# Kernel tuning notes

Hardware: AMD Instinct MI355X
Metric: run time of the kernel (lower is better)

## Reference

```python
import jax, jax.numpy as jnp
import numpy as np

N = 50000      # nodes
E = 800000     # random edges (self-loops appended -> E + N total)
IN, HID, OUT, HEADS = 128, 256, 256, 8


def _gat_layer(x, src, dst, W, a_src, a_dst, bias):
    # x: [N, F_in]; W: [F_in, H*C]; a_src/a_dst: [H, C]; bias: [H*C]
    n = x.shape[0]
    H, C = a_src.shape
    h = (x @ W).reshape(n, H, C)                      # per-head transform
    al_s = jnp.sum(h * a_src, axis=-1)                # [N, H]
    al_d = jnp.sum(h * a_dst, axis=-1)                # [N, H]
    e = jax.nn.leaky_relu(al_s[src] + al_d[dst], 0.2) # [E, H]
    # segmented softmax over incoming edges of each destination node
    m = jax.ops.segment_max(e, dst, num_segments=n)   # [N, H]
    e = jnp.exp(e - m[dst])
    s = jax.ops.segment_sum(e, dst, num_segments=n)   # [N, H]
    alpha = e / (s[dst] + 1e-16)                      # [E, H]
    out = jax.ops.segment_sum(alpha[:, :, None] * h[src], dst, num_segments=n)
    return out.reshape(n, H * C) + bias


def setup_inputs() -> dict:
    key = jax.random.key(0)
    ks = jax.random.split(key, 9)
    x = jax.random.normal(ks[0], (N, IN), dtype=jnp.float32)
    src = jax.random.randint(ks[1], (E,), 0, N)
    dst = jax.random.randint(ks[2], (E,), 0, N)
    loop = jnp.arange(N)  # PyG GATConv adds self-loops by default
    edge_index = jnp.stack([jnp.concatenate([src, loop]),
                            jnp.concatenate([dst, loop])]).astype(jnp.int64)
    C1, C2 = HID // HEADS, OUT // HEADS
    W1 = jax.random.normal(ks[3], (IN, HID), jnp.float32) * (1.0 / np.sqrt(IN))
    a1_src = jax.random.normal(ks[4], (HEADS, C1), jnp.float32) * 0.1
    a1_dst = jax.random.normal(ks[5], (HEADS, C1), jnp.float32) * 0.1
    b1 = jnp.zeros((HID,), jnp.float32)
    W2 = jax.random.normal(ks[6], (HID, OUT), jnp.float32) * (1.0 / np.sqrt(HID))
    a2_src = jax.random.normal(ks[7], (HEADS, C2), jnp.float32) * 0.1
    a2_dst = jax.random.normal(ks[8], (HEADS, C2), jnp.float32) * 0.1
    b2 = jnp.zeros((OUT,), jnp.float32)
    return {"x": x, "edge_index": edge_index,
            "W1": W1, "a1_src": a1_src, "a1_dst": a1_dst, "b1": b1,
            "W2": W2, "a2_src": a2_src, "a2_dst": a2_dst, "b2": b2}


def reference(x, edge_index, W1, a1_src, a1_dst, b1, W2, a2_src, a2_dst, b2):
    src, dst = edge_index[0], edge_index[1]
    h = jax.nn.elu(_gat_layer(x, src, dst, W1, a1_src, a1_dst, b1))
    out = jax.nn.elu(_gat_layer(h, src, dst, W2, a2_src, a2_dst, b2))
    return out
```

## Files before the change

kernel.cpp:

```cpp
#include <hip/hip_runtime.h>
#include <hip/hip_bf16.h>


#define HEADS 8
#define F 256

typedef _Float16 h8 __attribute__((ext_vector_type(8)));
typedef _Float16 h4 __attribute__((ext_vector_type(4)));
typedef float f4 __attribute__((ext_vector_type(4)));

#define WAVE_SYNC() do { __builtin_amdgcn_wave_barrier(); \
  asm volatile("s_waitcnt lgkmcnt(0)" ::: "memory"); \
  __builtin_amdgcn_wave_barrier(); } while (0)


__global__ void k_cvt(const float* __restrict__ in, _Float16* __restrict__ out, int n) {
  int i = blockIdx.x * blockDim.x + threadIdx.x;
  int idx = i * 4;
  if (idx < n) {
    float4 v = *(const float4*)&in[idx];
    h4 o = {(_Float16)v.x, (_Float16)v.y, (_Float16)v.z, (_Float16)v.w};
    *(h4*)&out[idx] = o;
  }
}

__global__ void k_cvt_wt(const float* __restrict__ W, _Float16* __restrict__ Wt, int K) {
  int k = blockIdx.x, n = threadIdx.x;
  Wt[(size_t)n * K + k] = (_Float16)W[(size_t)k * F + n];
}


__global__ void k_hist(const int* __restrict__ dst, int Et, int* __restrict__ deg) {
  int i = blockIdx.x * blockDim.x + threadIdx.x;
  if (i < Et) atomicAdd(&deg[dst[i]], 1);
}

__global__ __launch_bounds__(1024) void k_scan1(const int* __restrict__ deg, int n,
                                                int* __restrict__ rowptr, int* __restrict__ bsum) {
  __shared__ int s[1024];
  int i = blockIdx.x * 1024 + threadIdx.x;
  int v = (i < n) ? deg[i] : 0;
  s[threadIdx.x] = v;
  __syncthreads();
  for (int off = 1; off < 1024; off <<= 1) {
    int add = (threadIdx.x >= off) ? s[threadIdx.x - off] : 0;
    __syncthreads();
    s[threadIdx.x] += add;
    __syncthreads();
  }
  if (i < n) rowptr[i] = s[threadIdx.x] - v;
  if (threadIdx.x == 1023) bsum[blockIdx.x] = s[1023];
}

__global__ void k_scan2(const int* __restrict__ bsum, int nb, int* __restrict__ boff) {
  int t = threadIdx.x;
  int v = (t < nb) ? bsum[t] : 0;
  int inc = v;
  for (int off = 1; off < 64; off <<= 1) {
    int y = __shfl_up(inc, off, 64);
    if (t >= off) inc += y;
  }
  boff[t] = inc - v;
}

__global__ void k_scan3(int n, int Et, int* __restrict__ rowptr, const int* __restrict__ boff) {
  int i = blockIdx.x * blockDim.x + threadIdx.x;
  if (i < n) rowptr[i] += boff[i >> 10];
  if (i == 0) rowptr[n] = Et;
}

__global__ void k_fill(const int* __restrict__ src, const int* __restrict__ dst, int Et,
                       const int* __restrict__ rowptr, int* __restrict__ fill,
                       int* __restrict__ csr_src) {
  int i = blockIdx.x * blockDim.x + threadIdx.x;
  if (i < Et) {
    int d = dst[i];
    int pos = rowptr[d] + atomicAdd(&fill[d], 1);
    csr_src[pos] = src[i];
  }
}


__global__ __launch_bounds__(256) void k_gemm(const _Float16* __restrict__ A,
                                              const _Float16* __restrict__ Bt,
                                              _Float16* __restrict__ C,
                                              const float* __restrict__ a_src,
                                              const float* __restrict__ a_dst,
                                              float* __restrict__ als,
                                              float* __restrict__ ald,
                                              int M, int K) {
  __shared__ _Float16 As[64][40];
  __shared__ _Float16 Bs[256][40];
  int tid = threadIdx.x;
  int lane = tid & 63, w = tid >> 6;
  int rowBase = blockIdx.x * 64;
  f4 acc[4][4] = {};

  int arow = tid >> 2, akoff = (tid & 3) * 8;
  int arow_g = min(rowBase + arow, M - 1);
  const _Float16* Ap = A + (size_t)arow_g * K + akoff;
  const _Float16* Bp = Bt + (size_t)tid * K;

  int kl = (lane >> 4) * 8;
  int rl = lane & 15;

  for (int k0 = 0; k0 < K; k0 += 32) {
    h8 av = *(const h8*)(Ap + k0);
    h8 bv0 = *(const h8*)(Bp + k0);
    h8 bv1 = *(const h8*)(Bp + k0 + 8);
    h8 bv2 = *(const h8*)(Bp + k0 + 16);
    h8 bv3 = *(const h8*)(Bp + k0 + 24);
    *(h8*)&As[arow][akoff] = av;
    *(h8*)&Bs[tid][0] = bv0;
    *(h8*)&Bs[tid][8] = bv1;
    *(h8*)&Bs[tid][16] = bv2;
    *(h8*)&Bs[tid][24] = bv3;
    __syncthreads();
    h8 af[4], bf[4];
#pragma unroll
    for (int fi = 0; fi < 4; ++fi) af[fi] = *(const h8*)&As[fi * 16 + rl][kl];
#pragma unroll
    for (int fj = 0; fj < 4; ++fj) bf[fj] = *(const h8*)&Bs[w * 64 + fj * 16 + rl][kl];
#pragma unroll
    for (int fi = 0; fi < 4; ++fi)
#pragma unroll
      for (int fj = 0; fj < 4; ++fj)
        acc[fi][fj] = __builtin_amdgcn_mfma_f32_16x16x32_f16(af[fi], bf[fj], acc[fi][fj], 0, 0, 0);
    __syncthreads();
  }

  int rquad = (lane >> 4) * 4;

#pragma unroll
  for (int fi = 0; fi < 4; ++fi)
#pragma unroll
    for (int fj = 0; fj < 4; ++fj) {
      int col = w * 64 + fj * 16 + rl;
#pragma unroll
      for (int r = 0; r < 4; ++r) {
        int row = rowBase + fi * 16 + rquad + r;
        if (row < M) C[(size_t)row * F + col] = (_Float16)acc[fi][fj][r];
      }
    }

  int head0 = w * 2;
  float as0 = a_src[head0 * 32 + rl],      as1 = a_src[head0 * 32 + 16 + rl];
  float ad0 = a_dst[head0 * 32 + rl],      ad1 = a_dst[head0 * 32 + 16 + rl];
  float cs0 = a_src[head0 * 32 + 32 + rl], cs1 = a_src[head0 * 32 + 48 + rl];
  float cd0 = a_dst[head0 * 32 + 32 + rl], cd1 = a_dst[head0 * 32 + 48 + rl];
#pragma unroll
  for (int fi = 0; fi < 4; ++fi)
#pragma unroll
    for (int r = 0; r < 4; ++r) {
      float v0s = acc[fi][0][r] * as0 + acc[fi][1][r] * as1;
      float v0d = acc[fi][0][r] * ad0 + acc[fi][1][r] * ad1;
      float v1s = acc[fi][2][r] * cs0 + acc[fi][3][r] * cs1;
      float v1d = acc[fi][2][r] * cd0 + acc[fi][3][r] * cd1;
#pragma unroll
      for (int off = 8; off; off >>= 1) {
        v0s += __shfl_xor(v0s, off);
        v0d += __shfl_xor(v0d, off);
        v1s += __shfl_xor(v1s, off);
        v1d += __shfl_xor(v1d, off);
      }
      int row = rowBase + fi * 16 + rquad + r;
      if (rl == 0 && row < M) {
        als[row * HEADS + head0] = v0s;
        ald[row * HEADS + head0] = v0d;
        als[row * HEADS + head0 + 1] = v1s;
        ald[row * HEADS + head0 + 1] = v1d;
      }
    }
}


template <bool F16OUT>
__global__ __launch_bounds__(256) void k_agg(const int* __restrict__ rowptr,
                                             const int* __restrict__ csr_src,
                                             const float* __restrict__ al_s,
                                             const float* __restrict__ al_d,
                                             const _Float16* __restrict__ h,
                                             const float* __restrict__ bias,
                                             float* __restrict__ outf,
                                             _Float16* __restrict__ outh,
                                             int n) {
  __shared__ float eps[4][64][8];
  __shared__ int ssrc[4][64];
  int tid = threadIdx.x;
  int w = tid >> 6, lane = tid & 63;
  int node = blockIdx.x * 4 + w;
  if (node >= n) return;
  int base = rowptr[node];
  int d = rowptr[node + 1] - base;
  int hh = lane >> 3, slot = lane & 7;
  float alD = al_d[node * HEADS + hh];

  float invs;
  f4 facc = {0.f, 0.f, 0.f, 0.f};
  const _Float16* hc = h + (lane << 2);

  if (d <= 64) {
    float m = -1e30f;
    for (int j = slot; j < d; j += 8) {
      int s = csr_src[base + j];
      if (hh == 0) ssrc[w][j] = s;
      float e = al_s[s * HEADS + hh] + alD;
      e = (e > 0.f) ? e : 0.2f * e;
      eps[w][j][hh] = e;
      m = fmaxf(m, e);
    }
#pragma unroll
    for (int off = 4; off; off >>= 1) m = fmaxf(m, __shfl_xor(m, off));
    float sm = 0.f;
    for (int j = slot; j < d; j += 8) {
      float p = __expf(eps[w][j][hh] - m);
      eps[w][j][hh] = p;
      sm += p;
    }
#pragma unroll
    for (int off = 4; off; off >>= 1) sm += __shfl_xor(sm, off);
    invs = 1.f / (sm + 1e-16f);
    WAVE_SYNC();
    int j = 0;
    for (; j + 4 <= d; j += 4) {
      int s0 = __builtin_amdgcn_readfirstlane(ssrc[w][j]);
      int s1 = __builtin_amdgcn_readfirstlane(ssrc[w][j + 1]);
      int s2 = __builtin_amdgcn_readfirstlane(ssrc[w][j + 2]);
      int s3 = __builtin_amdgcn_readfirstlane(ssrc[w][j + 3]);
      float p0 = eps[w][j][hh], p1 = eps[w][j + 1][hh];
      float p2 = eps[w][j + 2][hh], p3 = eps[w][j + 3][hh];
      h4 v0 = *(const h4*)(hc + ((size_t)s0 << 8));
      h4 v1 = *(const h4*)(hc + ((size_t)s1 << 8));
      h4 v2 = *(const h4*)(hc + ((size_t)s2 << 8));
      h4 v3 = *(const h4*)(hc + ((size_t)s3 << 8));
      facc.x += p0 * (float)v0.x + p1 * (float)v1.x + p2 * (float)v2.x + p3 * (float)v3.x;
      facc.y += p0 * (float)v0.y + p1 * (float)v1.y + p2 * (float)v2.y + p3 * (float)v3.y;
      facc.z += p0 * (float)v0.z + p1 * (float)v1.z + p2 * (float)v2.z + p3 * (float)v3.z;
      facc.w += p0 * (float)v0.w + p1 * (float)v1.w + p2 * (float)v2.w + p3 * (float)v3.w;
    }
    for (; j < d; ++j) {
      int s0 = __builtin_amdgcn_readfirstlane(ssrc[w][j]);
      float p0 = eps[w][j][hh];
      h4 v0 = *(const h4*)(hc + ((size_t)s0 << 8));
      facc.x += p0 * (float)v0.x;
      facc.y += p0 * (float)v0.y;
      facc.z += p0 * (float)v0.z;
      facc.w += p0 * (float)v0.w;
    }
  } else {
    float m = -1e30f;
    for (int j = slot; j < d; j += 8) {
      int s = csr_src[base + j];
      float e = al_s[s * HEADS + hh] + alD;
      e = (e > 0.f) ? e : 0.2f * e;
      m = fmaxf(m, e);
    }
#pragma unroll
    for (int off = 4; off; off >>= 1) m = fmaxf(m, __shfl_xor(m, off));
    float sm = 0.f;
    for (int j = slot; j < d; j += 8) {
      int s = csr_src[base + j];
      float e = al_s[s * HEADS + hh] + alD;
      e = (e > 0.f) ? e : 0.2f * e;
      sm += __expf(e - m);
    }
#pragma unroll
    for (int off = 4; off; off >>= 1) sm += __shfl_xor(sm, off);
    invs = 1.f / (sm + 1e-16f);
    for (int c0 = 0; c0 < d; c0 += 64) {
      int cn = min(64, d - c0);
      WAVE_SYNC();
      for (int j = slot; j < cn; j += 8) {
        int s = csr_src[base + c0 + j];
        if (hh == 0) ssrc[w][j] = s;
        float e = al_s[s * HEADS + hh] + alD;
        e = (e > 0.f) ? e : 0.2f * e;
        eps[w][j][hh] = __expf(e - m);
      }
      WAVE_SYNC();
      for (int j = 0; j < cn; ++j) {
        int s0 = __builtin_amdgcn_readfirstlane(ssrc[w][j]);
        float p0 = eps[w][j][hh];
        h4 v0 = *(const h4*)(hc + ((size_t)s0 << 8));
        facc.x += p0 * (float)v0.x;
        facc.y += p0 * (float)v0.y;
        facc.z += p0 * (float)v0.z;
        facc.w += p0 * (float)v0.w;
      }
    }
  }

  int c0 = lane << 2;
  float4 bv = *(const float4*)&bias[c0];
  float o0 = facc.x * invs + bv.x;
  float o1 = facc.y * invs + bv.y;
  float o2 = facc.z * invs + bv.z;
  float o3 = facc.w * invs + bv.w;
  o0 = (o0 > 0.f) ? o0 : expm1f(o0);
  o1 = (o1 > 0.f) ? o1 : expm1f(o1);
  o2 = (o2 > 0.f) ? o2 : expm1f(o2);
  o3 = (o3 > 0.f) ? o3 : expm1f(o3);
  if (F16OUT) {
    h4 o = {(_Float16)o0, (_Float16)o1, (_Float16)o2, (_Float16)o3};
    *(h4*)&outh[((size_t)node << 8) + c0] = o;
  } else {
    *(float4*)&outf[((size_t)node << 8) + c0] = make_float4(o0, o1, o2, o3);
  }
}


extern "C" void kernel_launch(void* const* d_in, const int* in_sizes, int n_in,
                              void* d_out, int out_size, void* d_ws, size_t ws_size,
                              hipStream_t stream) {
  const float* x   = (const float*)d_in[0];
  const int*   ei  = (const int*)d_in[1];
  const float* W1  = (const float*)d_in[2];
  const float* a1s = (const float*)d_in[3];
  const float* a1d = (const float*)d_in[4];
  const float* b1  = (const float*)d_in[5];
  const float* W2  = (const float*)d_in[6];
  const float* a2s = (const float*)d_in[7];
  const float* a2d = (const float*)d_in[8];
  const float* b2  = (const float*)d_in[9];

  int n  = in_sizes[0] / 128;
  int Et = in_sizes[1] / 2;
  const int* srcp = ei;
  const int* dstp = ei + Et;

  char* ws = (char*)d_ws;
  auto alloc = [&](size_t bytes) {
    char* p = ws;
    ws += (bytes + 255) & ~(size_t)255;
    return p;
  };
  _Float16* xh     = (_Float16*)alloc((size_t)n * 128 * 2);
  _Float16* hbuf   = (_Float16*)alloc((size_t)n * F * 2);
  _Float16* Wt1    = (_Float16*)alloc((size_t)128 * F * 2);
  _Float16* Wt2    = (_Float16*)alloc((size_t)F * F * 2);
  float*    als    = (float*)alloc((size_t)n * HEADS * 4);
  float*    ald    = (float*)alloc((size_t)n * HEADS * 4);
  int*      deg    = (int*)alloc((size_t)n * 4);
  int*      fill   = (int*)alloc((size_t)n * 4);
  int*      rowptr = (int*)alloc((size_t)(n + 1) * 4);
  int*      bsum   = (int*)alloc(64 * 4);
  int*      boff   = (int*)alloc(64 * 4);
  int*      csr    = (int*)alloc((size_t)Et * 4);
  _Float16* out1h  = (_Float16*)d_out;
  float*    outF   = (float*)d_out;

  hipMemsetAsync(deg, 0, (size_t)n * 4, stream);
  hipMemsetAsync(fill, 0, (size_t)n * 4, stream);

  k_cvt<<<(n * 128 / 4 + 255) / 256, 256, 0, stream>>>(x, xh, n * 128);
  k_cvt_wt<<<128, 256, 0, stream>>>(W1, Wt1, 128);
  k_cvt_wt<<<256, 256, 0, stream>>>(W2, Wt2, 256);

  int eb = (Et + 255) / 256;
  k_hist<<<eb, 256, 0, stream>>>(dstp, Et, deg);
  int nb = (n + 1023) / 1024;
  k_scan1<<<nb, 1024, 0, stream>>>(deg, n, rowptr, bsum);
  k_scan2<<<1, 64, 0, stream>>>(bsum, nb, boff);
  k_scan3<<<(n + 255) / 256, 256, 0, stream>>>(n, Et, rowptr, boff);
  k_fill<<<eb, 256, 0, stream>>>(srcp, dstp, Et, rowptr, fill, csr);

  int gb = (n + 63) / 64;
  int ab = (n + 3) / 4;
  k_gemm<<<gb, 256, 0, stream>>>(xh, Wt1, hbuf, a1s, a1d, als, ald, n, 128);
  k_agg<true><<<ab, 256, 0, stream>>>(rowptr, csr, als, ald, hbuf, b1, nullptr, out1h, n);
  k_gemm<<<gb, 256, 0, stream>>>(out1h, Wt2, hbuf, a2s, a2d, als, ald, n, 256);
  k_agg<false><<<ab, 256, 0, stream>>>(rowptr, csr, als, ald, hbuf, b2, outF, nullptr, n);
}
```

Before: 395.3 us.

## Split attention aggregation into alpha and gather kernels, prefetch GEMM tiles

Splits the fused softmax+aggregation kernel into a kernel that writes normalized fp16 attention weights per edge and a separate gather kernel that reads them. It also register-prefetches the next K tile in the GEMM, merges the two weight-transpose launches, and drops the fill counter by atomically bumping a copy of rowptr. The split adds an extra Et*8 fp16 write and read per layer plus an extra launch. The fp16 alpha slightly reduces precision.

```diff
diff --git a/kernel.cpp b/kernel.cpp
--- a/kernel.cpp
+++ b/kernel.cpp
@@ -8,10 +8,6 @@
 typedef _Float16 h8 __attribute__((ext_vector_type(8)));
 typedef _Float16 h4 __attribute__((ext_vector_type(4)));
 typedef float f4 __attribute__((ext_vector_type(4)));
-
-#define WAVE_SYNC() do { __builtin_amdgcn_wave_barrier(); \
-  asm volatile("s_waitcnt lgkmcnt(0)" ::: "memory"); \
-  __builtin_amdgcn_wave_barrier(); } while (0)
 
 
 __global__ void k_cvt(const float* __restrict__ in, _Float16* __restrict__ out, int n) {
@@ -24,9 +20,14 @@
   }
 }
 
-__global__ void k_cvt_wt(const float* __restrict__ W, _Float16* __restrict__ Wt, int K) {
-  int k = blockIdx.x, n = threadIdx.x;
-  Wt[(size_t)n * K + k] = (_Float16)W[(size_t)k * F + n];
+__global__ void k_cvt_wt2(const float* __restrict__ W1, _Float16* __restrict__ Wt1,
+                          const float* __restrict__ W2, _Float16* __restrict__ Wt2) {
+  int b = blockIdx.x, n = threadIdx.x;
+  if (b < 128) Wt1[(size_t)n * 128 + b] = (_Float16)W1[(size_t)b * F + n];
+  else {
+    int k = b - 128;
+    Wt2[(size_t)n * 256 + k] = (_Float16)W2[(size_t)k * F + n];
+  }
 }
 
 
@@ -63,19 +64,22 @@
   boff[t] = inc - v;
 }
 
-__global__ void k_scan3(int n, int Et, int* __restrict__ rowptr, const int* __restrict__ boff) {
+__global__ void k_scan3(int n, int Et, int* __restrict__ rowptr,
+                        int* __restrict__ rowwork, const int* __restrict__ boff) {
   int i = blockIdx.x * blockDim.x + threadIdx.x;
-  if (i < n) rowptr[i] += boff[i >> 10];
+  if (i < n) {
+    int v = rowptr[i] + boff[i >> 10];
+    rowptr[i] = v;
+    rowwork[i] = v;
+  }
   if (i == 0) rowptr[n] = Et;
 }
 
 __global__ void k_fill(const int* __restrict__ src, const int* __restrict__ dst, int Et,
-                       const int* __restrict__ rowptr, int* __restrict__ fill,
-                       int* __restrict__ csr_src) {
+                       int* __restrict__ rowwork, int* __restrict__ csr_src) {
   int i = blockIdx.x * blockDim.x + threadIdx.x;
   if (i < Et) {
-    int d = dst[i];
-    int pos = rowptr[d] + atomicAdd(&fill[d], 1);
+    int pos = atomicAdd(&rowwork[dst[i]], 1);
     csr_src[pos] = src[i];
   }
 }
@@ -104,18 +108,28 @@
   int kl = (lane >> 4) * 8;
   int rl = lane & 15;
 
-  for (int k0 = 0; k0 < K; k0 += 32) {
-    h8 av = *(const h8*)(Ap + k0);
-    h8 bv0 = *(const h8*)(Bp + k0);
-    h8 bv1 = *(const h8*)(Bp + k0 + 8);
-    h8 bv2 = *(const h8*)(Bp + k0 + 16);
-    h8 bv3 = *(const h8*)(Bp + k0 + 24);
+  int nsteps = K >> 5;
+  h8 av = *(const h8*)(Ap);
+  h8 bv0 = *(const h8*)(Bp);
+  h8 bv1 = *(const h8*)(Bp + 8);
+  h8 bv2 = *(const h8*)(Bp + 16);
+  h8 bv3 = *(const h8*)(Bp + 24);
+
+  for (int s = 0; s < nsteps; ++s) {
     *(h8*)&As[arow][akoff] = av;
     *(h8*)&Bs[tid][0] = bv0;
     *(h8*)&Bs[tid][8] = bv1;
     *(h8*)&Bs[tid][16] = bv2;
     *(h8*)&Bs[tid][24] = bv3;
     __syncthreads();
+    if (s + 1 < nsteps) {
+      int k0 = (s + 1) << 5;
+      av = *(const h8*)(Ap + k0);
+      bv0 = *(const h8*)(Bp + k0);
+      bv1 = *(const h8*)(Bp + k0 + 8);
+      bv2 = *(const h8*)(Bp + k0 + 16);
+      bv3 = *(const h8*)(Bp + k0 + 24);
+    }
     h8 af[4], bf[4];
 #pragma unroll
     for (int fi = 0; fi < 4; ++fi) af[fi] = *(const h8*)&As[fi * 16 + rl][kl];
@@ -174,18 +188,13 @@
 }
 
 
-template <bool F16OUT>
-__global__ __launch_bounds__(256) void k_agg(const int* __restrict__ rowptr,
-                                             const int* __restrict__ csr_src,
-                                             const float* __restrict__ al_s,
-                                             const float* __restrict__ al_d,
-                                             const _Float16* __restrict__ h,
-                                             const float* __restrict__ bias,
-                                             float* __restrict__ outf,
-                                             _Float16* __restrict__ outh,
-                                             int n) {
+__global__ __launch_bounds__(256) void k_alpha(const int* __restrict__ rowptr,
+                                               const int* __restrict__ csr_src,
+                                               const float* __restrict__ al_s,
+                                               const float* __restrict__ al_d,
+                                               _Float16* __restrict__ alpha,
+                                               int n) {
   __shared__ float eps[4][64][8];
-  __shared__ int ssrc[4][64];
   int tid = threadIdx.x;
   int w = tid >> 6, lane = tid & 63;
   int node = blockIdx.x * 4 + w;
@@ -195,15 +204,10 @@
   int hh = lane >> 3, slot = lane & 7;
   float alD = al_d[node * HEADS + hh];
 
-  float invs;
-  f4 facc = {0.f, 0.f, 0.f, 0.f};
-  const _Float16* hc = h + (lane << 2);
-
   if (d <= 64) {
     float m = -1e30f;
     for (int j = slot; j < d; j += 8) {
       int s = csr_src[base + j];
-      if (hh == 0) ssrc[w][j] = s;
       float e = al_s[s * HEADS + hh] + alD;
       e = (e > 0.f) ? e : 0.2f * e;
       eps[w][j][hh] = e;
@@ -219,34 +223,9 @@
     }
 #pragma unroll
     for (int off = 4; off; off >>= 1) sm += __shfl_xor(sm, off);
-    invs = 1.f / (sm + 1e-16f);
-    WAVE_SYNC();
-    int j = 0;
-    for (; j + 4 <= d; j += 4) {
-      int s0 = __builtin_amdgcn_readfirstlane(ssrc[w][j]);
-      int s1 = __builtin_amdgcn_readfirstlane(ssrc[w][j + 1]);
-      int s2 = __builtin_amdgcn_readfirstlane(ssrc[w][j + 2]);
-      int s3 = __builtin_amdgcn_readfirstlane(ssrc[w][j + 3]);
-      float p0 = eps[w][j][hh], p1 = eps[w][j + 1][hh];
-      float p2 = eps[w][j + 2][hh], p3 = eps[w][j + 3][hh];
-      h4 v0 = *(const h4*)(hc + ((size_t)s0 << 8));
-      h4 v1 = *(const h4*)(hc + ((size_t)s1 << 8));
-      h4 v2 = *(const h4*)(hc + ((size_t)s2 << 8));
-      h4 v3 = *(const h4*)(hc + ((size_t)s3 << 8));
-      facc.x += p0 * (float)v0.x + p1 * (float)v1.x + p2 * (float)v2.x + p3 * (float)v3.x;
-      facc.y += p0 * (float)v0.y + p1 * (float)v1.y + p2 * (float)v2.y + p3 * (float)v3.y;
-      facc.z += p0 * (float)v0.z + p1 * (float)v1.z + p2 * (float)v2.z + p3 * (float)v3.z;
-      facc.w += p0 * (float)v0.w + p1 * (float)v1.w + p2 * (float)v2.w + p3 * (float)v3.w;
-    }
-    for (; j < d; ++j) {
-      int s0 = __builtin_amdgcn_readfirstlane(ssrc[w][j]);
-      float p0 = eps[w][j][hh];
-      h4 v0 = *(const h4*)(hc + ((size_t)s0 << 8));
-      facc.x += p0 * (float)v0.x;
-      facc.y += p0 * (float)v0.y;
-      facc.z += p0 * (float)v0.z;
-      facc.w += p0 * (float)v0.w;
-    }
+    float invs = 1.f / (sm + 1e-16f);
+    for (int j = slot; j < d; j += 8)
+      alpha[(size_t)(base + j) * 8 + hh] = (_Float16)(eps[w][j][hh] * invs);
   } else {
     float m = -1e30f;
     for (int j = slot; j < d; j += 8) {
@@ -266,36 +245,74 @@
     }
 #pragma unroll
     for (int off = 4; off; off >>= 1) sm += __shfl_xor(sm, off);
-    invs = 1.f / (sm + 1e-16f);
-    for (int c0 = 0; c0 < d; c0 += 64) {
-      int cn = min(64, d - c0);
-      WAVE_SYNC();
-      for (int j = slot; j < cn; j += 8) {
-        int s = csr_src[base + c0 + j];
-        if (hh == 0) ssrc[w][j] = s;
-        float e = al_s[s * HEADS + hh] + alD;
-        e = (e > 0.f) ? e : 0.2f * e;
-        eps[w][j][hh] = __expf(e - m);
-      }
-      WAVE_SYNC();
-      for (int j = 0; j < cn; ++j) {
-        int s0 = __builtin_amdgcn_readfirstlane(ssrc[w][j]);
-        float p0 = eps[w][j][hh];
-        h4 v0 = *(const h4*)(hc + ((size_t)s0 << 8));
-        facc.x += p0 * (float)v0.x;
-        facc.y += p0 * (float)v0.y;
-        facc.z += p0 * (float)v0.z;
-        facc.w += p0 * (float)v0.w;
-      }
-    }
+    float invs = 1.f / (sm + 1e-16f);
+    for (int j = slot; j < d; j += 8) {
+      int s = csr_src[base + j];
+      float e = al_s[s * HEADS + hh] + alD;
+      e = (e > 0.f) ? e : 0.2f * e;
+      alpha[(size_t)(base + j) * 8 + hh] = (_Float16)(__expf(e - m) * invs);
+    }
+  }
+}
+
+
+template <bool F16OUT>
+__global__ __launch_bounds__(256) void k_gather(const int* __restrict__ rowptr,
+                                                const int* __restrict__ csr_src,
+                                                const _Float16* __restrict__ alpha,
+                                                const _Float16* __restrict__ h,
+                                                const float* __restrict__ bias,
+                                                float* __restrict__ outf,
+                                                _Float16* __restrict__ outh,
+                                                int n) {
+  int tid = threadIdx.x;
+  int w = tid >> 6, lane = tid & 63;
+  int node = blockIdx.x * 4 + w;
+  if (node >= n) return;
+  int base = rowptr[node];
+  int d = rowptr[node + 1] - base;
+  int hh = lane >> 3;
+  const _Float16* hc = h + (lane << 2);
+  const _Float16* ap = alpha + hh;
+  f4 acc = {0.f, 0.f, 0.f, 0.f};
+
+  int j = 0;
+  for (; j + 4 <= d; j += 4) {
+    size_t e0 = base + j;
+    int s0 = __builtin_amdgcn_readfirstlane(csr_src[e0]);
+    int s1 = __builtin_amdgcn_readfirstlane(csr_src[e0 + 1]);
+    int s2 = __builtin_amdgcn_readfirstlane(csr_src[e0 + 2]);
+    int s3 = __builtin_amdgcn_readfirstlane(csr_src[e0 + 3]);
+    float a0 = (float)ap[e0 * 8];
+    float a1 = (float)ap[(e0 + 1) * 8];
+    float a2 = (float)ap[(e0 + 2) * 8];
+    float a3 = (float)ap[(e0 + 3) * 8];
+    h4 v0 = *(const h4*)(hc + ((size_t)s0 << 8));
+    h4 v1 = *(const h4*)(hc + ((size_t)s1 << 8));
+    h4 v2 = *(const h4*)(hc + ((size_t)s2 << 8));
+    h4 v3 = *(const h4*)(hc + ((size_t)s3 << 8));
+    acc.x += a0 * (float)v0.x + a1 * (float)v1.x + a2 * (float)v2.x + a3 * (float)v3.x;
+    acc.y += a0 * (float)v0.y + a1 * (float)v1.y + a2 * (float)v2.y + a3 * (float)v3.y;
+    acc.z += a0 * (float)v0.z + a1 * (float)v1.z + a2 * (float)v2.z + a3 * (float)v3.z;
+    acc.w += a0 * (float)v0.w + a1 * (float)v1.w + a2 * (float)v2.w + a3 * (float)v3.w;
+  }
+  for (; j < d; ++j) {
+    size_t e0 = base + j;
+    int s0 = __builtin_amdgcn_readfirstlane(csr_src[e0]);
+    float a0 = (float)ap[e0 * 8];
+    h4 v0 = *(const h4*)(hc + ((size_t)s0 << 8));
+    acc.x += a0 * (float)v0.x;
+    acc.y += a0 * (float)v0.y;
+    acc.z += a0 * (float)v0.z;
+    acc.w += a0 * (float)v0.w;
   }
 
   int c0 = lane << 2;
   float4 bv = *(const float4*)&bias[c0];
-  float o0 = facc.x * invs + bv.x;
-  float o1 = facc.y * invs + bv.y;
-  float o2 = facc.z * invs + bv.z;
-  float o3 = facc.w * invs + bv.w;
+  float o0 = acc.x + bv.x;
+  float o1 = acc.y + bv.y;
+  float o2 = acc.z + bv.z;
+  float o3 = acc.w + bv.w;
   o0 = (o0 > 0.f) ? o0 : expm1f(o0);
   o1 = (o1 > 0.f) ? o1 : expm1f(o1);
   o2 = (o2 > 0.f) ? o2 : expm1f(o2);
@@ -334,40 +351,41 @@
     ws += (bytes + 255) & ~(size_t)255;
     return p;
   };
-  _Float16* xh     = (_Float16*)alloc((size_t)n * 128 * 2);
-  _Float16* hbuf   = (_Float16*)alloc((size_t)n * F * 2);
-  _Float16* Wt1    = (_Float16*)alloc((size_t)128 * F * 2);
-  _Float16* Wt2    = (_Float16*)alloc((size_t)F * F * 2);
-  float*    als    = (float*)alloc((size_t)n * HEADS * 4);
-  float*    ald    = (float*)alloc((size_t)n * HEADS * 4);
-  int*      deg    = (int*)alloc((size_t)n * 4);
-  int*      fill   = (int*)alloc((size_t)n * 4);
-  int*      rowptr = (int*)alloc((size_t)(n + 1) * 4);
-  int*      bsum   = (int*)alloc(64 * 4);
-  int*      boff   = (int*)alloc(64 * 4);
-  int*      csr    = (int*)alloc((size_t)Et * 4);
-  _Float16* out1h  = (_Float16*)d_out;
-  float*    outF   = (float*)d_out;
+  _Float16* xh      = (_Float16*)alloc((size_t)n * 128 * 2);
+  _Float16* hbuf    = (_Float16*)alloc((size_t)n * F * 2);
+  _Float16* Wt1     = (_Float16*)alloc((size_t)128 * F * 2);
+  _Float16* Wt2     = (_Float16*)alloc((size_t)F * F * 2);
+  _Float16* alpha   = (_Float16*)alloc((size_t)Et * HEADS * 2);
+  float*    als     = (float*)alloc((size_t)n * HEADS * 4);
+  float*    ald     = (float*)alloc((size_t)n * HEADS * 4);
+  int*      deg     = (int*)alloc((size_t)n * 4);
+  int*      rowptr  = (int*)alloc((size_t)(n + 1) * 4);
+  int*      rowwork = (int*)alloc((size_t)n * 4);
+  int*      bsum    = (int*)alloc(64 * 4);
+  int*      boff    = (int*)alloc(64 * 4);
+  int*      csr     = (int*)alloc((size_t)Et * 4);
+  _Float16* out1h   = (_Float16*)d_out;
+  float*    outF    = (float*)d_out;
 
   hipMemsetAsync(deg, 0, (size_t)n * 4, stream);
-  hipMemsetAsync(fill, 0, (size_t)n * 4, stream);
 
   k_cvt<<<(n * 128 / 4 + 255) / 256, 256, 0, stream>>>(x, xh, n * 128);
-  k_cvt_wt<<<128, 256, 0, stream>>>(W1, Wt1, 128);
-  k_cvt_wt<<<256, 256, 0, stream>>>(W2, Wt2, 256);
+  k_cvt_wt2<<<384, 256, 0, stream>>>(W1, Wt1, W2, Wt2);
 
   int eb = (Et + 255) / 256;
   k_hist<<<eb, 256, 0, stream>>>(dstp, Et, deg);
   int nb = (n + 1023) / 1024;
   k_scan1<<<nb, 1024, 0, stream>>>(deg, n, rowptr, bsum);
   k_scan2<<<1, 64, 0, stream>>>(bsum, nb, boff);
-  k_scan3<<<(n + 255) / 256, 256, 0, stream>>>(n, Et, rowptr, boff);
-  k_fill<<<eb, 256, 0, stream>>>(srcp, dstp, Et, rowptr, fill, csr);
+  k_scan3<<<(n + 255) / 256, 256, 0, stream>>>(n, Et, rowptr, rowwork, boff);
+  k_fill<<<eb, 256, 0, stream>>>(srcp, dstp, Et, rowwork, csr);
 
   int gb = (n + 63) / 64;
   int ab = (n + 3) / 4;
   k_gemm<<<gb, 256, 0, stream>>>(xh, Wt1, hbuf, a1s, a1d, als, ald, n, 128);
-  k_agg<true><<<ab, 256, 0, stream>>>(rowptr, csr, als, ald, hbuf, b1, nullptr, out1h, n);
+  k_alpha<<<ab, 256, 0, stream>>>(rowptr, csr, als, ald, alpha, n);
+  k_gather<true><<<ab, 256, 0, stream>>>(rowptr, csr, alpha, hbuf, b1, nullptr, out1h, n);
   k_gemm<<<gb, 256, 0, stream>>>(out1h, Wt2, hbuf, a2s, a2d, als, ald, n, 256);
-  k_agg<false><<<ab, 256, 0, stream>>>(rowptr, csr, als, ald, hbuf, b2, outF, nullptr, n);
-}
+  k_alpha<<<ab, 256, 0, stream>>>(rowptr, csr, als, ald, alpha, n);
+  k_gather<false><<<ab, 256, 0, stream>>>(rowptr, csr, alpha, hbuf, b2, outF, nullptr, n);
+}
```

After: 421.5 us. +6.6%, slower.

## Fuse prep kernels, drop fill buffer, enlarge GEMM tile with register prefetch

Applied to the files above, without the earlier changes.

Merges the x conversion, both weight transposes and the degree histogram into one launch. The CSR fill now takes positions by atomic increment of a copy of rowptr, which removes the separate fill array and its memset. The GEMM now computes 128-row tiles with 512 threads laid out as 2x4 waves, and it prefetches the next k-slice into registers while the MFMAs run on the current one. These changes target launch overhead, B-tile reloading across blocks and global load latency, at the cost of more registers and fewer GEMM blocks.

```diff
diff --git a/kernel.cpp b/kernel.cpp
--- a/kernel.cpp
+++ b/kernel.cpp
@@ -14,26 +14,32 @@
   __builtin_amdgcn_wave_barrier(); } while (0)
 
 
-__global__ void k_cvt(const float* __restrict__ in, _Float16* __restrict__ out, int n) {
-  int i = blockIdx.x * blockDim.x + threadIdx.x;
-  int idx = i * 4;
-  if (idx < n) {
-    float4 v = *(const float4*)&in[idx];
-    h4 o = {(_Float16)v.x, (_Float16)v.y, (_Float16)v.z, (_Float16)v.w};
-    *(h4*)&out[idx] = o;
-  }
-}
-
-__global__ void k_cvt_wt(const float* __restrict__ W, _Float16* __restrict__ Wt, int K) {
-  int k = blockIdx.x, n = threadIdx.x;
-  Wt[(size_t)n * K + k] = (_Float16)W[(size_t)k * F + n];
-}
-
-
-__global__ void k_hist(const int* __restrict__ dst, int Et, int* __restrict__ deg) {
-  int i = blockIdx.x * blockDim.x + threadIdx.x;
-  if (i < Et) atomicAdd(&deg[dst[i]], 1);
-}
+__global__ void k_prep(const float* __restrict__ x, _Float16* __restrict__ xh, int n128,
+                       const float* __restrict__ W1, _Float16* __restrict__ Wt1,
+                       const float* __restrict__ W2, _Float16* __restrict__ Wt2,
+                       const int* __restrict__ dst, int Et, int* __restrict__ deg,
+                       int cvtB) {
+  int b = blockIdx.x, tid = threadIdx.x;
+  if (b < cvtB) {
+    int idx = (b * 256 + tid) * 4;
+    if (idx < n128) {
+      float4 v = *(const float4*)&x[idx];
+      h4 o = {(_Float16)v.x, (_Float16)v.y, (_Float16)v.z, (_Float16)v.w};
+      *(h4*)&xh[idx] = o;
+    }
+  } else if (b < cvtB + 384) {
+    int k = b - cvtB;
+    if (k < 128) Wt1[(size_t)tid * 128 + k] = (_Float16)W1[(size_t)k * F + tid];
+    else {
+      k -= 128;
+      Wt2[(size_t)tid * 256 + k] = (_Float16)W2[(size_t)k * F + tid];
+    }
+  } else {
+    int i = (b - cvtB - 384) * 256 + tid;
+    for (; i < Et; i += 512 * 256) atomicAdd(&deg[dst[i]], 1);
+  }
+}
+
 
 __global__ __launch_bounds__(1024) void k_scan1(const int* __restrict__ deg, int n,
                                                 int* __restrict__ rowptr, int* __restrict__ bsum) {
@@ -63,25 +69,28 @@
   boff[t] = inc - v;
 }
 
-__global__ void k_scan3(int n, int Et, int* __restrict__ rowptr, const int* __restrict__ boff) {
+__global__ void k_scan3(int n, int Et, int* __restrict__ rowptr,
+                        int* __restrict__ rowwork, const int* __restrict__ boff) {
   int i = blockIdx.x * blockDim.x + threadIdx.x;
-  if (i < n) rowptr[i] += boff[i >> 10];
+  if (i < n) {
+    int v = rowptr[i] + boff[i >> 10];
+    rowptr[i] = v;
+    rowwork[i] = v;
+  }
   if (i == 0) rowptr[n] = Et;
 }
 
 __global__ void k_fill(const int* __restrict__ src, const int* __restrict__ dst, int Et,
-                       const int* __restrict__ rowptr, int* __restrict__ fill,
-                       int* __restrict__ csr_src) {
+                       int* __restrict__ rowwork, int* __restrict__ csr_src) {
   int i = blockIdx.x * blockDim.x + threadIdx.x;
   if (i < Et) {
-    int d = dst[i];
-    int pos = rowptr[d] + atomicAdd(&fill[d], 1);
+    int pos = atomicAdd(&rowwork[dst[i]], 1);
     csr_src[pos] = src[i];
   }
 }
 
 
-__global__ __launch_bounds__(256) void k_gemm(const _Float16* __restrict__ A,
+__global__ __launch_bounds__(512) void k_gemm(const _Float16* __restrict__ A,
                                               const _Float16* __restrict__ Bt,
                                               _Float16* __restrict__ C,
                                               const float* __restrict__ a_src,
@@ -89,38 +98,44 @@
                                               float* __restrict__ als,
                                               float* __restrict__ ald,
                                               int M, int K) {
-  __shared__ _Float16 As[64][40];
+  __shared__ _Float16 As[128][40];
   __shared__ _Float16 Bs[256][40];
   int tid = threadIdx.x;
   int lane = tid & 63, w = tid >> 6;
-  int rowBase = blockIdx.x * 64;
+  int wr = w & 1, wc = w >> 1;
+  int rowBase = blockIdx.x * 128;
   f4 acc[4][4] = {};
 
   int arow = tid >> 2, akoff = (tid & 3) * 8;
   int arow_g = min(rowBase + arow, M - 1);
   const _Float16* Ap = A + (size_t)arow_g * K + akoff;
-  const _Float16* Bp = Bt + (size_t)tid * K;
+  int bc = tid >> 1, bkoff = (tid & 1) * 16;
+  const _Float16* Bp = Bt + (size_t)bc * K + bkoff;
 
   int kl = (lane >> 4) * 8;
   int rl = lane & 15;
 
-  for (int k0 = 0; k0 < K; k0 += 32) {
-    h8 av = *(const h8*)(Ap + k0);
-    h8 bv0 = *(const h8*)(Bp + k0);
-    h8 bv1 = *(const h8*)(Bp + k0 + 8);
-    h8 bv2 = *(const h8*)(Bp + k0 + 16);
-    h8 bv3 = *(const h8*)(Bp + k0 + 24);
+  int nsteps = K >> 5;
+  h8 av = *(const h8*)(Ap);
+  h8 bv0 = *(const h8*)(Bp);
+  h8 bv1 = *(const h8*)(Bp + 8);
+
+  for (int s = 0; s < nsteps; ++s) {
     *(h8*)&As[arow][akoff] = av;
-    *(h8*)&Bs[tid][0] = bv0;
-    *(h8*)&Bs[tid][8] = bv1;
-    *(h8*)&Bs[tid][16] = bv2;
-    *(h8*)&Bs[tid][24] = bv3;
+    *(h8*)&Bs[bc][bkoff] = bv0;
+    *(h8*)&Bs[bc][bkoff + 8] = bv1;
     __syncthreads();
+    if (s + 1 < nsteps) {
+      int k0 = (s + 1) << 5;
+      av = *(const h8*)(Ap + k0);
+      bv0 = *(const h8*)(Bp + k0);
+      bv1 = *(const h8*)(Bp + k0 + 8);
+    }
     h8 af[4], bf[4];
 #pragma unroll
-    for (int fi = 0; fi < 4; ++fi) af[fi] = *(const h8*)&As[fi * 16 + rl][kl];
-#pragma unroll
-    for (int fj = 0; fj < 4; ++fj) bf[fj] = *(const h8*)&Bs[w * 64 + fj * 16 + rl][kl];
+    for (int fi = 0; fi < 4; ++fi) af[fi] = *(const h8*)&As[wr * 64 + fi * 16 + rl][kl];
+#pragma unroll
+    for (int fj = 0; fj < 4; ++fj) bf[fj] = *(const h8*)&Bs[wc * 64 + fj * 16 + rl][kl];
 #pragma unroll
     for (int fi = 0; fi < 4; ++fi)
 #pragma unroll
@@ -135,15 +150,15 @@
   for (int fi = 0; fi < 4; ++fi)
 #pragma unroll
     for (int fj = 0; fj < 4; ++fj) {
-      int col = w * 64 + fj * 16 + rl;
+      int col = wc * 64 + fj * 16 + rl;
 #pragma unroll
       for (int r = 0; r < 4; ++r) {
-        int row = rowBase + fi * 16 + rquad + r;
+        int row = rowBase + wr * 64 + fi * 16 + rquad + r;
         if (row < M) C[(size_t)row * F + col] = (_Float16)acc[fi][fj][r];
       }
     }
 
-  int head0 = w * 2;
+  int head0 = wc * 2;
   float as0 = a_src[head0 * 32 + rl],      as1 = a_src[head0 * 32 + 16 + rl];
   float ad0 = a_dst[head0 * 32 + rl],      ad1 = a_dst[head0 * 32 + 16 + rl];
   float cs0 = a_src[head0 * 32 + 32 + rl], cs1 = a_src[head0 * 32 + 48 + rl];
@@ -163,7 +178,7 @@
         v1s += __shfl_xor(v1s, off);
         v1d += __shfl_xor(v1d, off);
       }
-      int row = rowBase + fi * 16 + rquad + r;
+      int row = rowBase + wr * 64 + fi * 16 + rquad + r;
       if (rl == 0 && row < M) {
         als[row * HEADS + head0] = v0s;
         ald[row * HEADS + head0] = v0d;
@@ -334,40 +349,38 @@
     ws += (bytes + 255) & ~(size_t)255;
     return p;
   };
-  _Float16* xh     = (_Float16*)alloc((size_t)n * 128 * 2);
-  _Float16* hbuf   = (_Float16*)alloc((size_t)n * F * 2);
-  _Float16* Wt1    = (_Float16*)alloc((size_t)128 * F * 2);
-  _Float16* Wt2    = (_Float16*)alloc((size_t)F * F * 2);
-  float*    als    = (float*)alloc((size_t)n * HEADS * 4);
-  float*    ald    = (float*)alloc((size_t)n * HEADS * 4);
-  int*      deg    = (int*)alloc((size_t)n * 4);
-  int*      fill   = (int*)alloc((size_t)n * 4);
-  int*      rowptr = (int*)alloc((size_t)(n + 1) * 4);
-  int*      bsum   = (int*)alloc(64 * 4);
-  int*      boff   = (int*)alloc(64 * 4);
-  int*      csr    = (int*)alloc((size_t)Et * 4);
-  _Float16* out1h  = (_Float16*)d_out;
-  float*    outF   = (float*)d_out;
+  _Float16* xh      = (_Float16*)alloc((size_t)n * 128 * 2);
+  _Float16* hbuf    = (_Float16*)alloc((size_t)n * F * 2);
+  _Float16* Wt1     = (_Float16*)alloc((size_t)128 * F * 2);
+  _Float16* Wt2     = (_Float16*)alloc((size_t)F * F * 2);
+  float*    als     = (float*)alloc((size_t)n * HEADS * 4);
+  float*    ald     = (float*)alloc((size_t)n * HEADS * 4);
+  int*      deg     = (int*)alloc((size_t)n * 4);
+  int*      rowptr  = (int*)alloc((size_t)(n + 1) * 4);
+  int*      rowwork = (int*)alloc((size_t)n * 4);
+  int*      bsum    = (int*)alloc(64 * 4);
+  int*      boff    = (int*)alloc(64 * 4);
+  int*      csr     = (int*)alloc((size_t)Et * 4);
+  _Float16* out1h   = (_Float16*)d_out;
+  float*    outF    = (float*)d_out;
 
   hipMemsetAsync(deg, 0, (size_t)n * 4, stream);
-  hipMemsetAsync(fill, 0, (size_t)n * 4, stream);
-
-  k_cvt<<<(n * 128 / 4 + 255) / 256, 256, 0, stream>>>(x, xh, n * 128);
-  k_cvt_wt<<<128, 256, 0, stream>>>(W1, Wt1, 128);
-  k_cvt_wt<<<256, 256, 0, stream>>>(W2, Wt2, 256);
-
-  int eb = (Et + 255) / 256;
-  k_hist<<<eb, 256, 0, stream>>>(dstp, Et, deg);
+
+  int n128 = n * 128;
+  int cvtB = (n128 / 4 + 255) / 256;
+  k_prep<<<cvtB + 384 + 512, 256, 0, stream>>>(x, xh, n128, W1, Wt1, W2, Wt2,
+                                               dstp, Et, deg, cvtB);
+
   int nb = (n + 1023) / 1024;
   k_scan1<<<nb, 1024, 0, stream>>>(deg, n, rowptr, bsum);
   k_scan2<<<1, 64, 0, stream>>>(bsum, nb, boff);
-  k_scan3<<<(n + 255) / 256, 256, 0, stream>>>(n, Et, rowptr, boff);
-  k_fill<<<eb, 256, 0, stream>>>(srcp, dstp, Et, rowptr, fill, csr);
-
-  int gb = (n + 63) / 64;
+  k_scan3<<<(n + 255) / 256, 256, 0, stream>>>(n, Et, rowptr, rowwork, boff);
+  k_fill<<<(Et + 255) / 256, 256, 0, stream>>>(srcp, dstp, Et, rowwork, csr);
+
+  int gb = (n + 127) / 128;
   int ab = (n + 3) / 4;
-  k_gemm<<<gb, 256, 0, stream>>>(xh, Wt1, hbuf, a1s, a1d, als, ald, n, 128);
+  k_gemm<<<gb, 512, 0, stream>>>(xh, Wt1, hbuf, a1s, a1d, als, ald, n, 128);
   k_agg<true><<<ab, 256, 0, stream>>>(rowptr, csr, als, ald, hbuf, b1, nullptr, out1h, n);
-  k_gemm<<<gb, 256, 0, stream>>>(out1h, Wt2, hbuf, a2s, a2d, als, ald, n, 256);
+  k_gemm<<<gb, 512, 0, stream>>>(out1h, Wt2, hbuf, a2s, a2d, als, ald, n, 256);
   k_agg<false><<<ab, 256, 0, stream>>>(rowptr, csr, als, ald, hbuf, b2, outF, nullptr, n);
 }
```

After: 376.2 us. 4.8% less time.
